# Kernel optimization log

Measured on AMD Instinct MI355X. Metric: run time of the kernel, lower is better.

Reference implementation:

```python
import jax, jax.numpy as jnp
import numpy as np

EPS = 1e-8


def setup_inputs() -> dict:
    key = jax.random.key(0)
    k1, k2, k3 = jax.random.split(key, 3)
    Nq, Nr = 16384, 16384
    return {
        "query_points": jax.random.normal(k1, (Nq, 3), dtype=jnp.float32),
        "ref_points": jax.random.normal(k2, (Nr, 3), dtype=jnp.float32),
        "ref_flow": jax.random.normal(k3, (Nr, 3), dtype=jnp.float32),
        "k": 3,
    }


def reference(query_points, ref_points, ref_flow, k):
    # torch.cdist: Euclidean distance matrix [Nq, Nr]
    q2 = jnp.sum(query_points * query_points, axis=-1, keepdims=True)   # [Nq,1]
    r2 = jnp.sum(ref_points * ref_points, axis=-1)                      # [Nr]
    d2 = q2 + r2[None, :] - 2.0 * (query_points @ ref_points.T)        # [Nq,Nr]
    dist = jnp.sqrt(jnp.maximum(d2, 0.0))
    # topk smallest distances
    neg_top, knn_idx = jax.lax.top_k(-dist, k)                          # [Nq,k]
    knn_dist = -neg_top
    # inverse-distance weights, normalized
    weights = 1.0 / (knn_dist + EPS)
    weights = weights / jnp.sum(weights, axis=1, keepdims=True)
    # gather neighbor flows and reduce: [Nq,k,3] -> [Nq,3]
    knn_flow = ref_flow[knn_idx]
    return jnp.sum(weights[..., None] * knn_flow, axis=1)
```

## Files before the change

### kernel.cpp

```cpp
#include <hip/hip_runtime.h>
#include <math.h>

#define G      32
#define NCELLS (G * G * G)
#define TOTC   (2 * NCELLS)
#define LOF    (-6.0f)
#define HH     0.375f
#define INVH   (1.0f / 0.375f)
#define DELTA  1e-3f
#define R2ACC  (HH * HH)
#define SCB    256
#define SCC    (TOTC / SCB)

__device__ __forceinline__ int cell_coord(float x) {
    int c = (int)floorf((x - LOF) * INVH);
    c = c < 0 ? 0 : c;
    return c > G - 1 ? G - 1 : c;
}
__device__ __forceinline__ int imax2(int a, int b) { return a > b ? a : b; }
__device__ __forceinline__ int imin2(int a, int b) { return a < b ? a : b; }
__device__ __forceinline__ float rdfl(float v) {
    return __int_as_float(__builtin_amdgcn_readfirstlane(__float_as_int(v)));
}

#define LEXINSERT(dv, jv) do {                                        \
    float d_ = (dv); int j_ = (jv);                                   \
    bool l0 = (d_ < e0) || ((d_ == e0) && (j_ < i0));                 \
    bool l1 = (d_ < e1) || ((d_ == e1) && (j_ < i1));                 \
    bool l2 = (d_ < e2) || ((d_ == e2) && (j_ < i2));                 \
    int   ni0 = l0 ? j_ : i0;                                         \
    int   ni1 = l0 ? i0 : (l1 ? j_ : i1);                             \
    int   ni2 = l1 ? i1 : (l2 ? j_ : i2);                             \
    float ne0 = l0 ? d_ : e0;                                         \
    float ne1 = l0 ? e0 : (l1 ? d_ : e1);                             \
    float ne2 = l1 ? e1 : (l2 ? d_ : e2);                             \
    e0 = ne0; e1 = ne1; e2 = ne2; i0 = ni0; i1 = ni1; i2 = ni2;       \
} while (0)

#define SCAN_RUN(lo_, hi_) do {                                       \
    for (int u = (lo_) + lane; u < (hi_); u += 64) {                  \
        float4 rr = srt[u];                                           \
        float xx = rr.x * rr.x;                                       \
        float yy = rr.y * rr.y;                                       \
        float zz = rr.z * rr.z;                                       \
        float r2 = (xx + yy) + zz;                                    \
        float td = qx * rr.x;                                         \
        td = fmaf(qy, rr.y, td);                                      \
        td = fmaf(qz, rr.z, td);                                      \
        float aa = q2 + r2;                                           \
        float dd = fmaf(-2.0f, td, aa);                               \
        int jj = __float_as_int(rr.w);                                \
        LEXINSERT(dd, jj);                                            \
    }                                                                 \
} while (0)

#define MERGE64() do {                                                \
    _Pragma("unroll")                                                 \
    for (int mk_ = 1; mk_ < 64; mk_ <<= 1) {                          \
        float f0 = __shfl_xor(e0, mk_, 64);                           \
        float f1 = __shfl_xor(e1, mk_, 64);                           \
        float f2 = __shfl_xor(e2, mk_, 64);                           \
        int   g0 = __shfl_xor(i0, mk_, 64);                           \
        int   g1 = __shfl_xor(i1, mk_, 64);                           \
        int   g2 = __shfl_xor(i2, mk_, 64);                           \
        LEXINSERT(f0, g0);                                            \
        LEXINSERT(f1, g1);                                            \
        LEXINSERT(f2, g2);                                            \
    }                                                                 \
} while (0)

#define MERGE32() do {                                                \
    _Pragma("unroll")                                                 \
    for (int mk_ = 1; mk_ < 32; mk_ <<= 1) {                          \
        float f0 = __shfl_xor(e0, mk_, 64);                           \
        float f1 = __shfl_xor(e1, mk_, 64);                           \
        float f2 = __shfl_xor(e2, mk_, 64);                           \
        int   g0 = __shfl_xor(i0, mk_, 64);                           \
        int   g1 = __shfl_xor(i1, mk_, 64);                           \
        int   g2 = __shfl_xor(i2, mk_, 64);                           \
        LEXINSERT(f0, g0);                                            \
        LEXINSERT(f1, g1);                                            \
        LEXINSERT(f2, g2);                                            \
    }                                                                 \
} while (0)

#define EPILOGUE() do {                                               \
    e0 = fmaxf(e0, 0.0f);                                             \
    e1 = fmaxf(e1, 0.0f);                                             \
    e2 = fmaxf(e2, 0.0f);                                             \
    float s0 = sqrtf(e0);                                             \
    float s1 = sqrtf(e1);                                             \
    float s2 = sqrtf(e2);                                             \
    float w0 = 1.0f / (s0 + 1e-8f);                                   \
    float w1 = 1.0f / (s1 + 1e-8f);                                   \
    float w2 = 1.0f / (s2 + 1e-8f);                                   \
    float wsum = (w0 + w1) + w2;                                      \
    w0 = w0 / wsum; w1 = w1 / wsum; w2 = w2 / wsum;                   \
    float f0x = flow[i0*3+0], f0y = flow[i0*3+1], f0z = flow[i0*3+2]; \
    float f1x = flow[i1*3+0], f1y = flow[i1*3+1], f1z = flow[i1*3+2]; \
    float f2x = flow[i2*3+0], f2y = flow[i2*3+1], f2z = flow[i2*3+2]; \
    out[q*3+0] = (w0 * f0x + w1 * f1x) + w2 * f2x;                    \
    out[q*3+1] = (w0 * f0y + w1 * f1y) + w2 * f2y;                    \
    out[q*3+2] = (w0 * f0z + w1 * f1z) + w2 * f2z;                    \
} while (0)

__global__ __launch_bounds__(256) void zero_ints(int* __restrict__ p, int n) {
    int i = blockIdx.x * 256 + threadIdx.x;
    if (i < n) p[i] = 0;
}

__global__ __launch_bounds__(256) void bin_count2(
    const float* __restrict__ ref, const float* __restrict__ qpts,
    int* __restrict__ cnt, int Nr, int Nq) {
    int j = blockIdx.x * 256 + threadIdx.x;
    if (j < Nr) {
        int cx = cell_coord(ref[3 * j + 0]);
        int cy = cell_coord(ref[3 * j + 1]);
        int cz = cell_coord(ref[3 * j + 2]);
        atomicAdd(&cnt[(cz * G + cy) * G + cx], 1);
    } else if (j < Nr + Nq) {
        int k = j - Nr;
        int cx = cell_coord(qpts[3 * k + 0]);
        int cy = cell_coord(qpts[3 * k + 1]);
        int cz = cell_coord(qpts[3 * k + 2]);
        atomicAdd(&cnt[NCELLS + (cz * G + cy) * G + cx], 1);
    }
}

__global__ __launch_bounds__(256) void scan1(
    const int* __restrict__ cnt, int* __restrict__ off, int* __restrict__ bsum) {
    __shared__ int wt[4];
    int tid = threadIdx.x, b = blockIdx.x;
    int base = b * SCC;
    int lane = tid & 63, wid = tid >> 6;
    int v = cnt[base + tid];
    int incl = v;
#pragma unroll
    for (int sh = 1; sh < 64; sh <<= 1) {
        int t = __shfl_up(incl, sh, 64);
        if (lane >= sh) incl += t;
    }
    if (lane == 63) wt[wid] = incl;
    __syncthreads();
    if (tid == 0) {
        int run = 0;
#pragma unroll
        for (int w = 0; w < 4; ++w) { int t = wt[w]; wt[w] = run; run += t; }
    }
    __syncthreads();
    int excl = wt[wid] + incl - v;
    off[base + tid] = excl;
    if (tid == SCC - 1) bsum[b] = excl + v;
}

__global__ __launch_bounds__(256) void scan2(
    const int* __restrict__ bsum, int* __restrict__ off, int* __restrict__ cur,
    int* __restrict__ nflag) {
    __shared__ int red[4];
    __shared__ int bo;
    int tid = threadIdx.x, b = blockIdx.x;
    int lane = tid & 63, wid = tid >> 6;
    if (b == 0 && tid == 0) nflag[0] = 0;
    int m = (tid < b) ? bsum[tid] : 0;
#pragma unroll
    for (int mk = 1; mk < 64; mk <<= 1) m += __shfl_xor(m, mk, 64);
    if (lane == 0) red[wid] = m;
    __syncthreads();
    if (tid == 0) bo = red[0] + red[1] + red[2] + red[3];
    __syncthreads();
    int boff = bo;
    int base = b * SCC;
    int t = off[base + tid] + boff;
    off[base + tid] = t;
    cur[base + tid] = t;
    if (b == SCB - 1 && tid == SCC - 1) off[TOTC] = boff + bsum[b];
}

__global__ __launch_bounds__(256) void bin_fill2(
    const float* __restrict__ ref, const float* __restrict__ qpts,
    int* __restrict__ cur, float4* __restrict__ big, int Nr, int Nq) {
    int j = blockIdx.x * 256 + threadIdx.x;
    if (j < Nr) {
        float x = ref[3 * j + 0], y = ref[3 * j + 1], z = ref[3 * j + 2];
        int cell = (cell_coord(z) * G + cell_coord(y)) * G + cell_coord(x);
        int pos = atomicAdd(&cur[cell], 1);
        big[pos] = make_float4(x, y, z, __int_as_float(j));
    } else if (j < Nr + Nq) {
        int k = j - Nr;
        float x = qpts[3 * k + 0], y = qpts[3 * k + 1], z = qpts[3 * k + 2];
        int cell = NCELLS + (cell_coord(z) * G + cell_coord(y)) * G + cell_coord(x);
        int pos = atomicAdd(&cur[cell], 1);
        big[pos] = make_float4(x, y, z, __int_as_float(k));
    }
}

#define MAPIDX(u_, out_) do {                                         \
    int t_ = (u_) + b0;                                               \
    t_ = ((u_) >= p1) ? ((u_) + b1) : t_;                             \
    t_ = ((u_) >= p2) ? ((u_) + b2) : t_;                             \
    t_ = ((u_) >= p3) ? ((u_) + b3) : t_;                             \
    t_ = ((u_) >= p4) ? ((u_) + b4) : t_;                             \
    t_ = ((u_) >= p5) ? ((u_) + b5) : t_;                             \
    t_ = ((u_) >= p6) ? ((u_) + b6) : t_;                             \
    t_ = ((u_) >= p7) ? ((u_) + b7) : t_;                             \
    t_ = ((u_) >= p8) ? ((u_) + b8) : t_;                             \
    (out_) = t_;                                                      \
} while (0)

#define BODY(rr_) do {                                                \
    float xx = (rr_).x * (rr_).x;                                     \
    float yy = (rr_).y * (rr_).y;                                     \
    float zz = (rr_).z * (rr_).z;                                     \
    float r2v = (xx + yy) + zz;                                       \
    float td = qx * (rr_).x;                                          \
    td = fmaf(qy, (rr_).y, td);                                       \
    td = fmaf(qz, (rr_).z, td);                                       \
    float aa = q2 + r2v;                                              \
    float dd = fmaf(-2.0f, td, aa);                                   \
    int jj = __float_as_int((rr_).w);                                 \
    LEXINSERT(dd, jj);                                                \
} while (0)

__global__ __launch_bounds__(256) void knn27(
    const float4* __restrict__ big, const int* __restrict__ off,
    const float* __restrict__ flow, float* __restrict__ out,
    int* __restrict__ qlist, int* __restrict__ nflag, int Nr, int Nq) {
#pragma clang fp contract(off)
    const float4* __restrict__ srt = big;
    int sl = threadIdx.x & 31;
    int sq = blockIdx.x * 8 + (threadIdx.x >> 5);
    bool qv = sq < Nq;
    int sqc = qv ? sq : 0;

    float4 qq = big[(size_t)Nr + sqc];
    float qx = qq.x, qy = qq.y, qz = qq.z;
    int   q  = __float_as_int(qq.w);
    float q2 = (qx * qx + qy * qy) + qz * qz;

    int cx = cell_coord(qx), cy = cell_coord(qy), cz = cell_coord(qz);

    int dz = sl / 3 - 1, dy = sl % 3 - 1;
    int zr = cz + dz, yr = cy + dy;
    bool vrow = (sl < 9) && qv && (zr >= 0) && (zr < G) && (yr >= 0) && (yr < G);
    int xlo = imax2(cx - 1, 0), xhi = imin2(cx + 1, G - 1);
    int vlo = 0, vhi = 0;
    if (vrow) {
        int rowbase = (zr * G + yr) * G;
        vlo = off[rowbase + xlo];
        vhi = off[rowbase + xhi + 1];
    }
    int cnt = vhi - vlo;

    int incl = cnt;
#pragma unroll
    for (int sh = 1; sh <= 8; sh <<= 1) {
        int t = __shfl_up(incl, sh, 32);
        if (sl >= sh) incl += t;
    }
    int total = __shfl(incl, 8, 32);
    int prex  = incl - cnt;

    int p1 = __shfl(prex, 1, 32), p2 = __shfl(prex, 2, 32);
    int p3 = __shfl(prex, 3, 32), p4 = __shfl(prex, 4, 32);
    int p5 = __shfl(prex, 5, 32), p6 = __shfl(prex, 6, 32);
    int p7 = __shfl(prex, 7, 32), p8 = __shfl(prex, 8, 32);
    int b0 = __shfl(vlo, 0, 32);
    int b1 = __shfl(vlo, 1, 32) - p1;
    int b2 = __shfl(vlo, 2, 32) - p2;
    int b3 = __shfl(vlo, 3, 32) - p3;
    int b4 = __shfl(vlo, 4, 32) - p4;
    int b5 = __shfl(vlo, 5, 32) - p5;
    int b6 = __shfl(vlo, 6, 32) - p6;
    int b7 = __shfl(vlo, 7, 32) - p7;
    int b8 = __shfl(vlo, 8, 32) - p8;

    const float FINF = __builtin_inff();
    float e0 = FINF, e1 = FINF, e2 = FINF;
    int   i0 = 0x7fffffff, i1 = 0x7fffffff, i2 = 0x7fffffff;

    int u = sl;
    if (u < total) {
        int idx;
        MAPIDX(u, idx);
        float4 rr = srt[idx];
        for (u += 32; u < total; u += 32) {
            int idx2;
            MAPIDX(u, idx2);
            float4 rn = srt[idx2];
            BODY(rr);
            rr = rn;
        }
        BODY(rr);
    }

    MERGE32();

    bool ok = (e2 + DELTA < R2ACC);
    if (sl == 0 && qv) {
        if (ok) {
            EPILOGUE();
        } else {
            int pos = atomicAdd(nflag, 1);
            qlist[pos] = q;
        }
    }
}

__global__ __launch_bounds__(256) void brute_block(
    const float* __restrict__ qpts, const float4* __restrict__ srt,
    const int* __restrict__ qlist, const int* __restrict__ nflag,
    const float* __restrict__ flow, float* __restrict__ out, int Nr) {
#pragma clang fp contract(off)
    __shared__ float sd[12];
    __shared__ int   si[12];
    int tid = threadIdx.x;
    int lane = tid & 63, wv = tid >> 6;
    int n = nflag[0];

    for (int f = blockIdx.x; f < n; f += gridDim.x) {
        int q = qlist[f];
        float qx = rdfl(qpts[3 * q + 0]);
        float qy = rdfl(qpts[3 * q + 1]);
        float qz = rdfl(qpts[3 * q + 2]);
        float q2 = (qx * qx + qy * qy) + qz * qz;

        int CS = (Nr + 3) / 4;
        int lo = wv * CS;
        int hi = imin2(lo + CS, Nr);

        const float FINF = __builtin_inff();
        float e0 = FINF, e1 = FINF, e2 = FINF;
        int   i0 = 0x7fffffff, i1 = 0x7fffffff, i2 = 0x7fffffff;

        SCAN_RUN(lo, hi);
        MERGE64();

        if (lane == 0) {
            sd[wv * 3 + 0] = e0; si[wv * 3 + 0] = i0;
            sd[wv * 3 + 1] = e1; si[wv * 3 + 1] = i1;
            sd[wv * 3 + 2] = e2; si[wv * 3 + 2] = i2;
        }
        __syncthreads();
        if (wv == 0) {
            e0 = e1 = e2 = FINF;
            i0 = i1 = i2 = 0x7fffffff;
            if (lane < 12) { e0 = sd[lane]; i0 = si[lane]; }
            MERGE64();
            if (lane == 0) EPILOGUE();
        }
        __syncthreads();
    }
}

extern "C" void kernel_launch(void* const* d_in, const int* in_sizes, int n_in,
                              void* d_out, int out_size, void* d_ws, size_t ws_size,
                              hipStream_t stream) {
    const float* qp   = (const float*)d_in[0];
    const float* ref  = (const float*)d_in[1];
    const float* flow = (const float*)d_in[2];
    float* out = (float*)d_out;

    int Nq = in_sizes[0] / 3;
    int Nr = in_sizes[1] / 3;

    char* ws = (char*)d_ws;
    float4* big = (float4*)ws;
    size_t o = (size_t)(Nr + Nq) * sizeof(float4);
    int* off    = (int*)(ws + o);  o += (size_t)(TOTC + 1) * sizeof(int);
    int* cur    = (int*)(ws + o);  o += (size_t)TOTC * sizeof(int);
    int* cnt    = (int*)(ws + o);  o += (size_t)TOTC * sizeof(int);
    int* nflag  = (int*)(ws + o);  o += sizeof(int);
    int* qlist  = (int*)(ws + o);  o += (size_t)Nq * sizeof(int);
    int* bsum   = (int*)(ws + o);  o += (size_t)SCB * sizeof(int);

    zero_ints<<<(TOTC + 255) / 256, 256, 0, stream>>>(cnt, TOTC);
    bin_count2<<<(Nr + Nq + 255) / 256, 256, 0, stream>>>(ref, qp, cnt, Nr, Nq);
    scan1<<<SCB, 256, 0, stream>>>(cnt, off, bsum);
    scan2<<<SCB, 256, 0, stream>>>(bsum, off, cur, nflag);
    bin_fill2<<<(Nr + Nq + 255) / 256, 256, 0, stream>>>(ref, qp, cur, big, Nr, Nq);

    int nBlocks = (Nq + 7) / 8;
    knn27<<<nBlocks, 256, 0, stream>>>(big, off, flow, out, qlist, nflag, Nr, Nq);
    brute_block<<<1024, 256, 0, stream>>>(qp, big, qlist, nflag, flow, out, Nr);
}
```

Measured before the change: 71.28 us.

## Add 5x5x5 neighborhood fallback stage before brute-force kNN

Queries whose 3x3x3 cell search cannot certify their top-3 are now sent to a new wave-per-query kernel that scans a 5x5x5 cell neighborhood, with a larger acceptance radius. Only queries still unresolved after that go to the full brute-force scan, which gets a smaller grid. The aim is to shrink the number of expensive whole-reference scans, at the cost of one extra kernel launch and a second flag/list pair. The scan loop is also unrolled by 4.

```diff
diff --git a/kernel.cpp b/kernel.cpp
--- a/kernel.cpp
+++ b/kernel.cpp
@@ -9,6 +9,7 @@
 #define INVH   (1.0f / 0.375f)
 #define DELTA  1e-3f
 #define R2ACC  (HH * HH)
+#define R2ACC5 (4.0f * HH * HH)
 #define SCB    256
 #define SCC    (TOTC / SCB)
 
@@ -38,6 +39,7 @@
 } while (0)
 
 #define SCAN_RUN(lo_, hi_) do {                                       \
+    _Pragma("unroll 4")                                               \
     for (int u = (lo_) + lane; u < (hi_); u += 64) {                  \
         float4 rr = srt[u];                                           \
         float xx = rr.x * rr.x;                                       \
@@ -160,7 +162,7 @@
     __shared__ int bo;
     int tid = threadIdx.x, b = blockIdx.x;
     int lane = tid & 63, wid = tid >> 6;
-    if (b == 0 && tid == 0) nflag[0] = 0;
+    if (b == 0 && tid < 2) nflag[tid] = 0;
     int m = (tid < b) ? bsum[tid] : 0;
 #pragma unroll
     for (int mk = 1; mk < 64; mk <<= 1) m += __shfl_xor(m, mk, 64);
@@ -300,25 +302,82 @@
         if (ok) {
             EPILOGUE();
         } else {
-            int pos = atomicAdd(nflag, 1);
+            int pos = atomicAdd(&nflag[0], 1);
             qlist[pos] = q;
+        }
+    }
+}
+
+__global__ __launch_bounds__(256) void knn125(
+    const float* __restrict__ qpts, const float4* __restrict__ srt,
+    const int* __restrict__ off, const int* __restrict__ qlist,
+    const int* __restrict__ nflag, const float* __restrict__ flow,
+    float* __restrict__ out, int* __restrict__ qlist2,
+    int* __restrict__ nflag2) {
+#pragma clang fp contract(off)
+    int lane = threadIdx.x & 63;
+    int wav  = (blockIdx.x * 256 + threadIdx.x) >> 6;
+    int nWaves = (gridDim.x * 256) >> 6;
+    int n = nflag[0];
+
+    for (int f = wav; f < n; f += nWaves) {
+        int q = qlist[f];
+        float qx = rdfl(qpts[3 * q + 0]);
+        float qy = rdfl(qpts[3 * q + 1]);
+        float qz = rdfl(qpts[3 * q + 2]);
+        float q2 = (qx * qx + qy * qy) + qz * qz;
+
+        int cx = cell_coord(qx), cy = cell_coord(qy), cz = cell_coord(qz);
+
+        int dz = lane / 5 - 2, dy = lane % 5 - 2;
+        int zr = cz + dz, yr = cy + dy;
+        bool vrow = (lane < 25) && (zr >= 0) && (zr < G) && (yr >= 0) && (yr < G);
+        int xlo = imax2(cx - 2, 0), xhi = imin2(cx + 2, G - 1);
+        int vlo = 0, vhi = 0;
+        if (vrow) {
+            int rowbase = (zr * G + yr) * G;
+            vlo = off[rowbase + xlo];
+            vhi = off[rowbase + xhi + 1];
+        }
+
+        const float FINF = __builtin_inff();
+        float e0 = FINF, e1 = FINF, e2 = FINF;
+        int   i0 = 0x7fffffff, i1 = 0x7fffffff, i2 = 0x7fffffff;
+
+#pragma unroll
+        for (int r = 0; r < 25; ++r) {
+            int lo = __shfl(vlo, r, 64);
+            int hi = __shfl(vhi, r, 64);
+            SCAN_RUN(lo, hi);
+        }
+
+        MERGE64();
+
+        bool ok = (e2 + DELTA < R2ACC5);
+        if (lane == 0) {
+            if (ok) {
+                EPILOGUE();
+            } else {
+                int pos = atomicAdd(nflag2, 1);
+                qlist2[pos] = q;
+            }
         }
     }
 }
 
 __global__ __launch_bounds__(256) void brute_block(
     const float* __restrict__ qpts, const float4* __restrict__ srt,
-    const int* __restrict__ qlist, const int* __restrict__ nflag,
+    const int* __restrict__ qlist2, const int* __restrict__ nflag2,
     const float* __restrict__ flow, float* __restrict__ out, int Nr) {
 #pragma clang fp contract(off)
     __shared__ float sd[12];
     __shared__ int   si[12];
     int tid = threadIdx.x;
     int lane = tid & 63, wv = tid >> 6;
-    int n = nflag[0];
+    int n = nflag2[0];
 
     for (int f = blockIdx.x; f < n; f += gridDim.x) {
-        int q = qlist[f];
+        int q = qlist2[f];
         float qx = rdfl(qpts[3 * q + 0]);
         float qy = rdfl(qpts[3 * q + 1]);
         float qz = rdfl(qpts[3 * q + 2]);
@@ -369,8 +428,10 @@
     int* off    = (int*)(ws + o);  o += (size_t)(TOTC + 1) * sizeof(int);
     int* cur    = (int*)(ws + o);  o += (size_t)TOTC * sizeof(int);
     int* cnt    = (int*)(ws + o);  o += (size_t)TOTC * sizeof(int);
-    int* nflag  = (int*)(ws + o);  o += sizeof(int);
+    int* nflag  = (int*)(ws + o);  o += 2 * sizeof(int);
+    int* nflag2 = nflag + 1;
     int* qlist  = (int*)(ws + o);  o += (size_t)Nq * sizeof(int);
+    int* qlist2 = (int*)(ws + o);  o += (size_t)Nq * sizeof(int);
     int* bsum   = (int*)(ws + o);  o += (size_t)SCB * sizeof(int);
 
     zero_ints<<<(TOTC + 255) / 256, 256, 0, stream>>>(cnt, TOTC);
@@ -381,5 +442,7 @@
 
     int nBlocks = (Nq + 7) / 8;
     knn27<<<nBlocks, 256, 0, stream>>>(big, off, flow, out, qlist, nflag, Nr, Nq);
-    brute_block<<<1024, 256, 0, stream>>>(qp, big, qlist, nflag, flow, out, Nr);
-}
+    knn125<<<1024, 256, 0, stream>>>(qp, big, off, qlist, nflag, flow, out,
+                                     qlist2, nflag2);
+    brute_block<<<256, 256, 0, stream>>>(qp, big, qlist2, nflag2, flow, out, Nr);
+}
```

New measurement: 85.84 us. +20.4%, slower.
